# Kernel optimization log

Measured on AMD Instinct MI355X. Metric: run time of the kernel, lower is better.

Reference implementation:

```python
import jax, jax.numpy as jnp
import numpy as np

KH = KW = 3
K = KH * KW
PAD = 1


def conv3x3(x, w, b):
    # x: [B,C,H,W], w: [O,C,3,3], b: [O]
    y = jax.lax.conv_general_dilated(x, w, (1, 1), ((PAD, PAD), (PAD, PAD)),
                                     dimension_numbers=('NCHW', 'OIHW', 'NCHW'))
    return y + b[None, :, None, None]


def deform_conv(x, offsets, w, b):
    # torchvision DeformConv2d, stride=1, pad=1, dilation=1, groups=1, offset_groups=1
    # x: [B,C,H,W], offsets: [B,2*K,H,W] ordered (dy,dx) per kernel point, w: [O,C,3,3]
    B, C, H, W = x.shape
    O = w.shape[0]
    off = offsets.reshape(B, K, 2, H, W)
    dy, dx = off[:, :, 0], off[:, :, 1]                      # [B,K,H,W]
    kyy, kxx = jnp.meshgrid(jnp.arange(KH), jnp.arange(KW), indexing='ij')
    ky = kyy.reshape(K).astype(x.dtype)
    kx = kxx.reshape(K).astype(x.dtype)
    py = dy + ky[None, :, None, None] + jnp.arange(H, dtype=x.dtype)[None, None, :, None] - PAD
    px = dx + kx[None, :, None, None] + jnp.arange(W, dtype=x.dtype)[None, None, None, :] - PAD
    y0 = jnp.floor(py)
    x0 = jnp.floor(px)
    wy = (py - y0)[:, None]                                   # [B,1,K,H,W]
    wx = (px - x0)[:, None]
    y0i = y0.astype(jnp.int32)
    x0i = x0.astype(jnp.int32)
    xf = x.reshape(B, C, H * W)

    def gather(yi, xi):
        valid = (yi >= 0) & (yi < H) & (xi >= 0) & (xi < W)   # zero outside
        yc = jnp.clip(yi, 0, H - 1)
        xc = jnp.clip(xi, 0, W - 1)
        idx = (yc * W + xc).reshape(B, 1, K * H * W)
        g = jnp.take_along_axis(xf, idx, axis=2).reshape(B, C, K, H, W)
        return g * valid[:, None].astype(x.dtype)

    v00 = gather(y0i, x0i)
    v01 = gather(y0i, x0i + 1)
    v10 = gather(y0i + 1, x0i)
    v11 = gather(y0i + 1, x0i + 1)
    samp = (v00 * (1 - wy) * (1 - wx) + v01 * (1 - wy) * wx
            + v10 * wy * (1 - wx) + v11 * wy * wx)            # [B,C,K,H,W]
    out = jnp.einsum('bckhw,ock->bohw', samp, w.reshape(O, C, K))
    return out + b[None, :, None, None]


def deform_align(x, y, wo, bo, wd, bd):
    return deform_conv(x, conv3x3(y, wo, bo), wd, bd)


def setup_inputs() -> dict:
    key = jax.random.key(0)
    ks = jax.random.split(key, 16)
    inC, embedC = 64, 96
    B, H, W = 4, 96, 96
    s = 0.02
    d = {
        'x1': jax.random.normal(ks[0], (B, inC, H, W), jnp.float32),
        'y': jax.random.normal(ks[1], (B, inC, H, W), jnp.float32),
        # block 1: offset conv inC->2K, deform conv inC->embedC
        'wo1': jax.random.normal(ks[2], (2 * K, inC, 3, 3), jnp.float32) * s,
        'bo1': jnp.zeros((2 * K,), jnp.float32),
        'wd1': jax.random.normal(ks[3], (embedC, inC, 3, 3), jnp.float32) * s,
        'bd1': jnp.zeros((embedC,), jnp.float32),
        # block 2: embedC->2K, embedC->embedC
        'wo2': jax.random.normal(ks[4], (2 * K, embedC, 3, 3), jnp.float32) * s,
        'bo2': jnp.zeros((2 * K,), jnp.float32),
        'wd2': jax.random.normal(ks[5], (embedC, embedC, 3, 3), jnp.float32) * s,
        'bd2': jnp.zeros((embedC,), jnp.float32),
        # block 3: embedC->2K, embedC->inC
        'wo3': jax.random.normal(ks[6], (2 * K, embedC, 3, 3), jnp.float32) * s,
        'bo3': jnp.zeros((2 * K,), jnp.float32),
        'wd3': jax.random.normal(ks[7], (inC, embedC, 3, 3), jnp.float32) * s,
        'bd3': jnp.zeros((inC,), jnp.float32),
    }
    return d


def reference(x1, y, wo1, bo1, wd1, bd1, wo2, bo2, wd2, bd2, wo3, bo3, wd3, bd3):
    h = deform_align(x1, y, wo1, bo1, wd1, bd1)
    h = deform_align(h, h, wo2, bo2, wd2, bd2)
    h = deform_align(h, h, wo3, bo3, wd3, bd3)
    return h
```

## Files before the change

kernel.cpp:

```cpp
#include <hip/hip_runtime.h>

constexpr int B = 4, H = 96, W = 96, HW = H * W;
constexpr int NPIX = B * HW;
constexpr int KOFF = 18;

typedef _Float16 half8 __attribute__((ext_vector_type(8)));
typedef _Float16 half4 __attribute__((ext_vector_type(4)));
typedef float f32x4 __attribute__((ext_vector_type(4)));
typedef __attribute__((address_space(3))) _Float16 lf16;

__device__ __forceinline__ int iclamp(int v, int lo, int hi) {
  return v < lo ? lo : (v > hi ? hi : v);
}

struct Corners {
  int i00, i01, i10, i11;
  float w00, w01, w10, w11;
};

__device__ __forceinline__ Corners mk_corners(float py, float qx) {
  float fy = floorf(py), fx = floorf(qx);
  float wy = py - fy, wx = qx - fx;
  int y0 = (int)fy, x0 = (int)fx;
  int y1 = y0 + 1, x1 = x0 + 1;
  bool vy0 = (y0 >= 0) & (y0 < H);
  bool vy1 = (y1 >= 0) & (y1 < H);
  bool vx0 = (x0 >= 0) & (x0 < W);
  bool vx1 = (x1 >= 0) & (x1 < W);
  int r0 = iclamp(y0, 0, H - 1) * W;
  int r1 = iclamp(y1, 0, H - 1) * W;
  int c0 = iclamp(x0, 0, W - 1);
  int c1 = iclamp(x1, 0, W - 1);
  Corners cc;
  cc.i00 = r0 + c0; cc.i01 = r0 + c1; cc.i10 = r1 + c0; cc.i11 = r1 + c1;
  float a = 1.f - wy, bb = 1.f - wx;
  cc.w00 = a * bb * ((vy0 & vx0) ? 1.f : 0.f);
  cc.w01 = a * wx * ((vy0 & vx1) ? 1.f : 0.f);
  cc.w10 = wy * bb * ((vy1 & vx0) ? 1.f : 0.f);
  cc.w11 = wy * wx * ((vy1 & vx1) ? 1.f : 0.f);
  return cc;
}

__device__ __forceinline__ void gld_lds16(const _Float16* g, lf16* l) {
  __builtin_amdgcn_global_load_lds(
      (const __attribute__((address_space(1))) void*)g,
      (__attribute__((address_space(3))) void*)l, 16, 0, 0);
}

template <int NF>
__device__ __forceinline__ void stage_coop(const _Float16* wk, lf16* lb, int lane,
                                           int wid) {
#pragma unroll
  for (int i = 0; i < (NF + 3) / 4; ++i) {
    int f = i * 4 + wid;
    if (f < NF)
      gld_lds16(wk + (size_t)f * 512 + lane * 8, lb + f * 512);
  }
}

template <int KS>
__device__ __forceinline__ void load_corners(const _Float16* xb, int ch, const Corners& cc,
                                             half8 r[KS][4]) {
  const _Float16* p00 = xb + (size_t)cc.i00 * (KS * 32) + ch;
  const _Float16* p01 = xb + (size_t)cc.i01 * (KS * 32) + ch;
  const _Float16* p10 = xb + (size_t)cc.i10 * (KS * 32) + ch;
  const _Float16* p11 = xb + (size_t)cc.i11 * (KS * 32) + ch;
#pragma unroll
  for (int ks = 0; ks < KS; ++ks) {
    r[ks][0] = *(const half8*)(p00 + ks * 32);
    r[ks][1] = *(const half8*)(p01 + ks * 32);
    r[ks][2] = *(const half8*)(p10 + ks * 32);
    r[ks][3] = *(const half8*)(p11 + ks * 32);
  }
}

template <int KS>
__device__ __forceinline__ void interp_corners(const Corners& cc, half8 r[KS][4],
                                               half8 a[KS]) {
  _Float16 q00 = (_Float16)cc.w00, q01 = (_Float16)cc.w01;
  _Float16 q10 = (_Float16)cc.w10, q11 = (_Float16)cc.w11;
#pragma unroll
  for (int ks = 0; ks < KS; ++ks)
    a[ks] = r[ks][0] * q00 + r[ks][1] * q01 + r[ks][2] * q10 + r[ks][3] * q11;
}

template <int KS>
__device__ __forceinline__ void load_shift(const _Float16* xb, int ch, int h, int w,
                                           int ky, int kx, half8 a[KS]) {
  int yy = h + ky, xx = w + kx;
  bool v = (yy >= 0) & (yy < H) & (xx >= 0) & (xx < W);
  int yc = iclamp(yy, 0, H - 1), xc = iclamp(xx, 0, W - 1);
  const _Float16* pv = xb + (size_t)(yc * W + xc) * (KS * 32) + ch;
#pragma unroll
  for (int ks = 0; ks < KS; ++ks) {
    half8 r = *(const half8*)(pv + ks * 32);
    half8 z = {0, 0, 0, 0, 0, 0, 0, 0};
    a[ks] = v ? r : z;
  }
}

template <int KS, int NJ>
__device__ __forceinline__ void mfma_lds(const _Float16* lb, int lane,
                                         half8 a[KS], f32x4 acc[NJ]) {
#pragma unroll
  for (int ks = 0; ks < KS; ++ks)
#pragma unroll
    for (int j = 0; j < NJ; ++j) {
      half8 b = *(const half8*)(lb + (ks * NJ + j) * 512 + lane * 8);
      acc[j] = __builtin_amdgcn_mfma_f32_16x16x32_f16(a[ks], b, acc[j], 0, 0, 0);
    }
}

struct WAll {
  const float* src[6];
  _Float16* dst[6];
  int C[6], Osrc[6], OPAD[6], base[6];
};

__global__ void wfrag_all_kernel(WAll wa) {
  int bid = blockIdx.x;
  int s = 0;
#pragma unroll
  for (int i = 1; i < 6; ++i) s += (bid >= wa.base[i]) ? 1 : 0;
  int fid = bid - wa.base[s];
  int C = wa.C[s], Osrc = wa.Osrc[s], OPAD = wa.OPAD[s];
  const float* wsrc = wa.src[s];
  _Float16* wf = wa.dst[s];
  int KS = C / 32;
  int NJ = OPAD / 16;
  int lane = threadIdx.x;
  int j = fid % NJ;
  int ks = (fid / NJ) % KS;
  int k = fid / (NJ * KS);
  int o = j * 16 + (lane & 15);
  int c0 = ks * 32 + (lane >> 4) * 8;
  half8 v;
#pragma unroll
  for (int u = 0; u < 8; ++u)
    v[u] = (o < Osrc) ? (_Float16)wsrc[((size_t)o * C + c0 + u) * 9 + k] : (_Float16)0.f;
  *(half8*)(wf + ((size_t)fid * 64 + lane) * 8) = v;
}

__global__ __launch_bounds__(256) void repack2_kernel(const float* __restrict__ in0,
                                                      const float* __restrict__ in1,
                                                      _Float16* __restrict__ o0,
                                                      _Float16* __restrict__ o1) {
  constexpr int C = 64;
  const float* in = blockIdx.y ? in1 : in0;
  _Float16* outh = blockIdx.y ? o1 : o0;
  __shared__ float tile[64 * C];
  int t = threadIdx.x;
  int pix0 = blockIdx.x * 64;
  int b = pix0 / HW;
  int hw0 = pix0 - b * HW;
  int l = t & 63;
  for (int cc = t >> 6; cc < C; cc += 4)
    tile[cc * 64 + l] = in[((size_t)b * C + cc) * HW + hw0 + l];
  __syncthreads();
  int pl = t >> 2;
  int cq = t & 3;
  _Float16* op = outh + (size_t)(pix0 + pl) * C + cq * (C / 4);
#pragma unroll
  for (int c = 0; c < C / 4; c += 4) {
    half4 hv;
#pragma unroll
    for (int u = 0; u < 4; ++u) hv[u] = (_Float16)tile[(cq * (C / 4) + c + u) * 64 + pl];
    *(half4*)(op + c) = hv;
  }
}

template <int C, int O, bool WF32, bool WH>
__global__ __launch_bounds__(256, 1)
void stage_kernel(const _Float16* __restrict__ xoff, const _Float16* __restrict__ xdef,
                  const _Float16* __restrict__ wfo, const float* __restrict__ bo,
                  const _Float16* __restrict__ wfd, const float* __restrict__ bd,
                  float* __restrict__ out, _Float16* __restrict__ outh) {
  constexpr int KS = C / 32;
  constexpr int NJ = O / 16;
  constexpr int NFD = KS * NJ;
  constexpr int NFO = KS * 2;
  __shared__ _Float16 ldsB[2 * NFD * 512];
  __shared__ float lofs[64][KOFF];
  lf16* lb3 = (lf16*)ldsB;
  const int tid = threadIdx.x;
  const int wid = tid >> 6;
  const int lane = tid & 63;
  const int row = lane & 15;
  const int kgrp = lane >> 4;
  const int ch = kgrp * 8;
  const int chunk = (blockIdx.x & 7) * (int)(gridDim.x >> 3) + (blockIdx.x >> 3);
  const int px0 = chunk * 64 + wid * 16;
  const int b = px0 / HW;
  const int hw0 = px0 - b * HW;
  const int hwm = hw0 + row;
  const int h0 = hwm / W, w0 = hwm - h0 * W;
  const _Float16* xo = xoff + (size_t)b * HW * C;
  const _Float16* xd = xdef + (size_t)b * HW * C;

  {
    f32x4 aoc[2];
#pragma unroll
    for (int j = 0; j < 2; ++j) {
      int o = j * 16 + row;
      float bv = (o < KOFF) ? bo[o] : 0.f;
      aoc[j] = {bv, bv, bv, bv};
    }
    half8 a[KS], n[KS];
    stage_coop<NFO>(wfo, lb3, lane, wid);
    load_shift<KS>(xo, ch, h0, w0, -1, -1, a);
#pragma unroll
    for (int k = 0; k < 9; ++k) {
      __syncthreads();
      if (k < 8) {
        int kn = k + 1;
        stage_coop<NFO>(wfo + (size_t)kn * (NFO * 512),
                        lb3 + (kn & 1) * NFD * 512, lane, wid);
        load_shift<KS>(xo, ch, h0, w0, kn / 3 - 1, kn % 3 - 1, n);
      }
      mfma_lds<KS, 2>(ldsB + (k & 1) * NFD * 512, lane, a, aoc);
      if (k < 8) {
#pragma unroll
        for (int ks = 0; ks < KS; ++ks) a[ks] = n[ks];
      }
    }
#pragma unroll
    for (int j = 0; j < 2; ++j) {
      int o = j * 16 + row;
      if (o < KOFF) {
#pragma unroll
        for (int r = 0; r < 4; ++r) lofs[wid * 16 + kgrp * 4 + r][o] = aoc[j][r];
      }
    }
  }
  __syncthreads();

  const int prow = wid * 16 + row;
  const float hf = (float)(h0 - 1), wwf = (float)(w0 - 1);

  f32x4 acc[NJ];
#pragma unroll
  for (int j = 0; j < NJ; ++j) {
    float bv = bd[j * 16 + row];
    acc[j] = {bv, bv, bv, bv};
  }
  half8 a[KS];
  half8 r[KS][4], rn[KS][4];
  Corners ccur = mk_corners(lofs[prow][0] + hf, lofs[prow][1] + wwf);
  stage_coop<NFD>(wfd, lb3, lane, wid);
  load_corners<KS>(xd, ch, ccur, r);
#pragma unroll
  for (int k = 0; k < 9; ++k) {
    __syncthreads();
    if (k < 8) {
      int kn = k + 1;
      stage_coop<NFD>(wfd + (size_t)kn * (NFD * 512),
                      lb3 + (kn & 1) * NFD * 512, lane, wid);
      Corners cn = mk_corners(lofs[prow][2 * kn] + hf + (float)(kn / 3),
                              lofs[prow][2 * kn + 1] + wwf + (float)(kn % 3));
      load_corners<KS>(xd, ch, cn, rn);
      interp_corners<KS>(ccur, r, a);
      mfma_lds<KS, NJ>(ldsB + (k & 1) * NFD * 512, lane, a, acc);
      ccur = cn;
#pragma unroll
      for (int ks = 0; ks < KS; ++ks)
#pragma unroll
        for (int q = 0; q < 4; ++q) r[ks][q] = rn[ks][q];
    } else {
      interp_corners<KS>(ccur, r, a);
      mfma_lds<KS, NJ>(ldsB + (k & 1) * NFD * 512, lane, a, acc);
    }
  }
#pragma unroll
  for (int j = 0; j < NJ; ++j) {
    int o = j * 16 + row;
#pragma unroll
    for (int r2 = 0; r2 < 4; ++r2) {
      int p = px0 + kgrp * 4 + r2;
      if (WF32) out[((size_t)b * O + o) * HW + (p - b * HW)] = acc[j][r2];
      if (WH) outh[(size_t)p * O + o] = (_Float16)acc[j][r2];
    }
  }
}

extern "C" void kernel_launch(void* const* d_in, const int* in_sizes, int n_in,
                              void* d_out, int out_size, void* d_ws, size_t ws_size,
                              hipStream_t stream) {
  const float* x1  = (const float*)d_in[0];
  const float* y   = (const float*)d_in[1];
  const float* wo1 = (const float*)d_in[2];
  const float* bo1 = (const float*)d_in[3];
  const float* wd1 = (const float*)d_in[4];
  const float* bd1 = (const float*)d_in[5];
  const float* wo2 = (const float*)d_in[6];
  const float* bo2 = (const float*)d_in[7];
  const float* wd2 = (const float*)d_in[8];
  const float* bd2 = (const float*)d_in[9];
  const float* wo3 = (const float*)d_in[10];
  const float* bo3 = (const float*)d_in[11];
  const float* wd3 = (const float*)d_in[12];
  const float* bd3 = (const float*)d_in[13];
  float* out = (float*)d_out;

  char* p = (char*)d_ws;
  auto alloc = [&](size_t bytes) {
    char* r = p;
    p += (bytes + 255) & ~(size_t)255;
    return r;
  };
  _Float16* Wo1f = (_Float16*)alloc((size_t)9 * 2 * 2 * 512 * 2);
  _Float16* Wo2f = (_Float16*)alloc((size_t)9 * 3 * 2 * 512 * 2);
  _Float16* Wo3f = (_Float16*)alloc((size_t)9 * 3 * 2 * 512 * 2);
  _Float16* W1f  = (_Float16*)alloc((size_t)9 * 2 * 6 * 512 * 2);
  _Float16* W2f  = (_Float16*)alloc((size_t)9 * 3 * 6 * 512 * 2);
  _Float16* W3f  = (_Float16*)alloc((size_t)9 * 3 * 4 * 512 * 2);
  _Float16* x1h = (_Float16*)alloc((size_t)NPIX * 64 * 2);
  _Float16* yh  = (_Float16*)alloc((size_t)NPIX * 64 * 2);
  _Float16* h1h = (_Float16*)alloc((size_t)NPIX * 96 * 2);
  _Float16* h2h = (_Float16*)alloc((size_t)NPIX * 96 * 2);

  WAll wa;
  wa.src[0] = wo1; wa.dst[0] = Wo1f; wa.C[0] = 64; wa.Osrc[0] = 18; wa.OPAD[0] = 32;
  wa.src[1] = wo2; wa.dst[1] = Wo2f; wa.C[1] = 96; wa.Osrc[1] = 18; wa.OPAD[1] = 32;
  wa.src[2] = wo3; wa.dst[2] = Wo3f; wa.C[2] = 96; wa.Osrc[2] = 18; wa.OPAD[2] = 32;
  wa.src[3] = wd1; wa.dst[3] = W1f;  wa.C[3] = 64; wa.Osrc[3] = 96; wa.OPAD[3] = 96;
  wa.src[4] = wd2; wa.dst[4] = W2f;  wa.C[4] = 96; wa.Osrc[4] = 96; wa.OPAD[4] = 96;
  wa.src[5] = wd3; wa.dst[5] = W3f;  wa.C[5] = 96; wa.Osrc[5] = 64; wa.OPAD[5] = 64;
  int base = 0;
  for (int i = 0; i < 6; ++i) {
    wa.base[i] = base;
    base += 9 * (wa.C[i] / 32) * (wa.OPAD[i] / 16);
  }
  hipLaunchKernelGGL(wfrag_all_kernel, dim3(base), dim3(64), 0, stream, wa);
  hipLaunchKernelGGL(repack2_kernel, dim3(NPIX / 64, 2), dim3(256), 0, stream,
                     x1, y, x1h, yh);

  dim3 gs(NPIX / 64);
  dim3 wb(256);

  hipLaunchKernelGGL((stage_kernel<64, 96, false, true>), gs, wb, 0, stream,
                     yh, x1h, Wo1f, bo1, W1f, bd1, (float*)nullptr, h1h);
  hipLaunchKernelGGL((stage_kernel<96, 96, false, true>), gs, wb, 0, stream,
                     h1h, h1h, Wo2f, bo2, W2f, bd2, (float*)nullptr, h2h);
  hipLaunchKernelGGL((stage_kernel<96, 64, true, false>), gs, wb, 0, stream,
                     h2h, h2h, Wo3f, bo3, W3f, bd3, out, (_Float16*)nullptr);
}
```

Measured before the change: 121.4 us.

## Process two 16-pixel tiles per wave to reuse LDS weight fragments

Each wave now handles 32 pixels as two 16-row MFMA tiles. Each LDS weight fragment read feeds two MFMAs, which halves LDS traffic per output and halves the grid size. The deform loop is also restructured to interleave corner gathers and interpolation for the next kernel point with the MFMA halves of the current one. This raises register pressure and halves block count, which may reduce occupancy and latency hiding.

```diff
diff --git a/kernel.cpp b/kernel.cpp
--- a/kernel.cpp
+++ b/kernel.cpp
@@ -99,15 +99,17 @@
   }
 }
 
-template <int KS, int NJ>
-__device__ __forceinline__ void mfma_lds(const _Float16* lb, int lane,
-                                         half8 a[KS], f32x4 acc[NJ]) {
+template <int KS, int NJ, int J0, int J1>
+__device__ __forceinline__ void mfma_dual(const _Float16* lb, int lane,
+                                          half8 a0[KS], half8 a1[KS],
+                                          f32x4 acc0[NJ], f32x4 acc1[NJ]) {
 #pragma unroll
   for (int ks = 0; ks < KS; ++ks)
 #pragma unroll
-    for (int j = 0; j < NJ; ++j) {
+    for (int j = J0; j < J1; ++j) {
       half8 b = *(const half8*)(lb + (ks * NJ + j) * 512 + lane * 8);
-      acc[j] = __builtin_amdgcn_mfma_f32_16x16x32_f16(a[ks], b, acc[j], 0, 0, 0);
+      acc0[j] = __builtin_amdgcn_mfma_f32_16x16x32_f16(a0[ks], b, acc0[j], 0, 0, 0);
+      acc1[j] = __builtin_amdgcn_mfma_f32_16x16x32_f16(a1[ks], b, acc1[j], 0, 0, 0);
     }
 }
 
@@ -180,7 +182,7 @@
   constexpr int NFD = KS * NJ;
   constexpr int NFO = KS * 2;
   __shared__ _Float16 ldsB[2 * NFD * 512];
-  __shared__ float lofs[64][KOFF];
+  __shared__ float lofs[128][KOFF];
   lf16* lb3 = (lf16*)ldsB;
   const int tid = threadIdx.x;
   const int wid = tid >> 6;
@@ -189,25 +191,28 @@
   const int kgrp = lane >> 4;
   const int ch = kgrp * 8;
   const int chunk = (blockIdx.x & 7) * (int)(gridDim.x >> 3) + (blockIdx.x >> 3);
-  const int px0 = chunk * 64 + wid * 16;
+  const int px0 = chunk * 128 + wid * 32;
   const int b = px0 / HW;
   const int hw0 = px0 - b * HW;
-  const int hwm = hw0 + row;
-  const int h0 = hwm / W, w0 = hwm - h0 * W;
+  const int hwm0 = hw0 + row, hwm1 = hw0 + 16 + row;
+  const int h0 = hwm0 / W, w0 = hwm0 - h0 * W;
+  const int h1 = hwm1 / W, w1 = hwm1 - h1 * W;
   const _Float16* xo = xoff + (size_t)b * HW * C;
   const _Float16* xd = xdef + (size_t)b * HW * C;
 
   {
-    f32x4 aoc[2];
+    f32x4 aoc0[2], aoc1[2];
 #pragma unroll
     for (int j = 0; j < 2; ++j) {
       int o = j * 16 + row;
       float bv = (o < KOFF) ? bo[o] : 0.f;
-      aoc[j] = {bv, bv, bv, bv};
-    }
-    half8 a[KS], n[KS];
+      aoc0[j] = {bv, bv, bv, bv};
+      aoc1[j] = {bv, bv, bv, bv};
+    }
+    half8 a0[KS], a1[KS], n0[KS], n1[KS];
     stage_coop<NFO>(wfo, lb3, lane, wid);
-    load_shift<KS>(xo, ch, h0, w0, -1, -1, a);
+    load_shift<KS>(xo, ch, h0, w0, -1, -1, a0);
+    load_shift<KS>(xo, ch, h1, w1, -1, -1, a1);
 #pragma unroll
     for (int k = 0; k < 9; ++k) {
       __syncthreads();
@@ -215,12 +220,13 @@
         int kn = k + 1;
         stage_coop<NFO>(wfo + (size_t)kn * (NFO * 512),
                         lb3 + (kn & 1) * NFD * 512, lane, wid);
-        load_shift<KS>(xo, ch, h0, w0, kn / 3 - 1, kn % 3 - 1, n);
-      }
-      mfma_lds<KS, 2>(ldsB + (k & 1) * NFD * 512, lane, a, aoc);
+        load_shift<KS>(xo, ch, h0, w0, kn / 3 - 1, kn % 3 - 1, n0);
+        load_shift<KS>(xo, ch, h1, w1, kn / 3 - 1, kn % 3 - 1, n1);
+      }
+      mfma_dual<KS, 2, 0, 2>(ldsB + (k & 1) * NFD * 512, lane, a0, a1, aoc0, aoc1);
       if (k < 8) {
 #pragma unroll
-        for (int ks = 0; ks < KS; ++ks) a[ks] = n[ks];
+        for (int ks = 0; ks < KS; ++ks) { a0[ks] = n0[ks]; a1[ks] = n1[ks]; }
       }
     }
 #pragma unroll
@@ -228,46 +234,60 @@
       int o = j * 16 + row;
       if (o < KOFF) {
 #pragma unroll
-        for (int r = 0; r < 4; ++r) lofs[wid * 16 + kgrp * 4 + r][o] = aoc[j][r];
+        for (int r = 0; r < 4; ++r) {
+          lofs[wid * 32 + kgrp * 4 + r][o] = aoc0[j][r];
+          lofs[wid * 32 + 16 + kgrp * 4 + r][o] = aoc1[j][r];
+        }
       }
     }
   }
   __syncthreads();
 
-  const int prow = wid * 16 + row;
-  const float hf = (float)(h0 - 1), wwf = (float)(w0 - 1);
-
-  f32x4 acc[NJ];
+  const int prow0 = wid * 32 + row, prow1 = prow0 + 16;
+  const float hf0 = (float)(h0 - 1), wf0_ = (float)(w0 - 1);
+  const float hf1 = (float)(h1 - 1), wf1_ = (float)(w1 - 1);
+
+  f32x4 acc0[NJ], acc1[NJ];
 #pragma unroll
   for (int j = 0; j < NJ; ++j) {
     float bv = bd[j * 16 + row];
-    acc[j] = {bv, bv, bv, bv};
-  }
-  half8 a[KS];
-  half8 r[KS][4], rn[KS][4];
-  Corners ccur = mk_corners(lofs[prow][0] + hf, lofs[prow][1] + wwf);
+    acc0[j] = {bv, bv, bv, bv};
+    acc1[j] = {bv, bv, bv, bv};
+  }
+  half8 a0[KS], a1[KS], a0n[KS], a1n[KS];
+  half8 rn[KS][4];
   stage_coop<NFD>(wfd, lb3, lane, wid);
-  load_corners<KS>(xd, ch, ccur, r);
+  {
+    Corners c0 = mk_corners(lofs[prow0][0] + hf0, lofs[prow0][1] + wf0_);
+    load_corners<KS>(xd, ch, c0, rn);
+    interp_corners<KS>(c0, rn, a0);
+    Corners c1 = mk_corners(lofs[prow1][0] + hf1, lofs[prow1][1] + wf1_);
+    load_corners<KS>(xd, ch, c1, rn);
+    interp_corners<KS>(c1, rn, a1);
+  }
 #pragma unroll
   for (int k = 0; k < 9; ++k) {
     __syncthreads();
+    const _Float16* lbk = ldsB + (k & 1) * NFD * 512;
     if (k < 8) {
       int kn = k + 1;
       stage_coop<NFD>(wfd + (size_t)kn * (NFD * 512),
                       lb3 + (kn & 1) * NFD * 512, lane, wid);
-      Corners cn = mk_corners(lofs[prow][2 * kn] + hf + (float)(kn / 3),
-                              lofs[prow][2 * kn + 1] + wwf + (float)(kn % 3));
-      load_corners<KS>(xd, ch, cn, rn);
-      interp_corners<KS>(ccur, r, a);
-      mfma_lds<KS, NJ>(ldsB + (k & 1) * NFD * 512, lane, a, acc);
-      ccur = cn;
-#pragma unroll
-      for (int ks = 0; ks < KS; ++ks)
-#pragma unroll
-        for (int q = 0; q < 4; ++q) r[ks][q] = rn[ks][q];
+      float kyf = (float)(kn / 3), kxf = (float)(kn % 3);
+      Corners cn0 = mk_corners(lofs[prow0][2 * kn] + hf0 + kyf,
+                               lofs[prow0][2 * kn + 1] + wf0_ + kxf);
+      load_corners<KS>(xd, ch, cn0, rn);
+      mfma_dual<KS, NJ, 0, NJ / 2>(lbk, lane, a0, a1, acc0, acc1);
+      interp_corners<KS>(cn0, rn, a0n);
+      Corners cn1 = mk_corners(lofs[prow1][2 * kn] + hf1 + kyf,
+                               lofs[prow1][2 * kn + 1] + wf1_ + kxf);
+      load_corners<KS>(xd, ch, cn1, rn);
+      mfma_dual<KS, NJ, NJ / 2, NJ>(lbk, lane, a0, a1, acc0, acc1);
+      interp_corners<KS>(cn1, rn, a1n);
+#pragma unroll
+      for (int ks = 0; ks < KS; ++ks) { a0[ks] = a0n[ks]; a1[ks] = a1n[ks]; }
     } else {
-      interp_corners<KS>(ccur, r, a);
-      mfma_lds<KS, NJ>(ldsB + (k & 1) * NFD * 512, lane, a, acc);
+      mfma_dual<KS, NJ, 0, NJ>(lbk, lane, a0, a1, acc0, acc1);
     }
   }
 #pragma unroll
@@ -275,9 +295,16 @@
     int o = j * 16 + row;
 #pragma unroll
     for (int r2 = 0; r2 < 4; ++r2) {
-      int p = px0 + kgrp * 4 + r2;
-      if (WF32) out[((size_t)b * O + o) * HW + (p - b * HW)] = acc[j][r2];
-      if (WH) outh[(size_t)p * O + o] = (_Float16)acc[j][r2];
+      int p0 = px0 + kgrp * 4 + r2;
+      int p1 = p0 + 16;
+      if (WF32) {
+        out[((size_t)b * O + o) * HW + (p0 - b * HW)] = acc0[j][r2];
+        out[((size_t)b * O + o) * HW + (p1 - b * HW)] = acc1[j][r2];
+      }
+      if (WH) {
+        outh[(size_t)p0 * O + o] = (_Float16)acc0[j][r2];
+        outh[(size_t)p1 * O + o] = (_Float16)acc1[j][r2];
+      }
     }
   }
 }
@@ -334,7 +361,7 @@
   hipLaunchKernelGGL(repack2_kernel, dim3(NPIX / 64, 2), dim3(256), 0, stream,
                      x1, y, x1h, yh);
 
-  dim3 gs(NPIX / 64);
+  dim3 gs(NPIX / 128);
   dim3 wb(256);
 
   hipLaunchKernelGGL((stage_kernel<64, 96, false, true>), gs, wb, 0, stream,
```

After: 151.6 us. 24.9% more time.
